# Performance work log

Measured on AMD Instinct MI355X. Metric: run time of the kernel, lower is better.

Reference implementation:

```python
import jax, jax.numpy as jnp
import numpy as np

IN_DIM = 256
OUT_DIM = 64
N = 8192
ALPHA = 0.2  # LeakyReLU negative slope
NEG_BIG = -9e15


def setup_inputs() -> dict:
    key = jax.random.key(0)
    k_h, k_A, k_W, k_a = jax.random.split(key, 4)
    h = jax.random.normal(k_h, (N, IN_DIM), dtype=jnp.float32)
    A = jax.random.randint(k_A, (N, N), 0, 2, dtype=jnp.int32)
    # xavier_uniform with gain=1.414
    gain = 1.414
    lim_W = gain * np.sqrt(6.0 / (IN_DIM + OUT_DIM))
    W = jax.random.uniform(k_W, (IN_DIM, OUT_DIM), minval=-lim_W, maxval=lim_W, dtype=jnp.float32)
    lim_a = gain * np.sqrt(6.0 / (2 * OUT_DIM + 1))
    a = jax.random.uniform(k_a, (2 * OUT_DIM, 1), minval=-lim_a, maxval=lim_a, dtype=jnp.float32)
    return {"h": h, "A": A, "W": W, "a": a}


def reference(h, A, W, a):
    # Wh: [N, d]
    Wh = h @ W
    # e_ij = leakyrelu([Wh_i || Wh_j] . a) = leakyrelu(Wh_i.a1 + Wh_j.a2)
    # -> avoid the O(N^2 * 2d) concat; compute rank-1 decomposition directly.
    a1 = a[:OUT_DIM, 0]   # [d]
    a2 = a[OUT_DIM:, 0]   # [d]
    f1 = Wh @ a1          # [N] contribution of source node i
    f2 = Wh @ a2          # [N] contribution of target node j
    e = jax.nn.leaky_relu(f1[:, None] + f2[None, :], negative_slope=ALPHA)  # [N, N]
    e = jnp.where(A > 0, e, NEG_BIG)
    attention = jax.nn.softmax(e, axis=1)  # [N, N]
    # dropout=0.0 (eval mode): identity
    h_prime = attention @ Wh               # [N, d]
    return jax.nn.elu(h_prime)             # concat=True -> ELU
```

## Files before the change

### kernel.cpp

```cpp
#include <hip/hip_runtime.h>
#include <math.h>
#include <stdint.h>

#define NV 8192
#define KD 256
#define DD 64
#define ALPHA 0.2f
#define TI 64
#define CJ 128
#define BLK 512

typedef _Float16 half8 __attribute__((ext_vector_type(8)));
typedef float floatx4 __attribute__((ext_vector_type(4)));

#define OFF_WHT  0
#define OFF_F1   (DD * NV / 2)
#define OFF_F2   (OFF_F1 + NV)
#define OFF_PACC (OFF_F2 + NV)

__global__ __launch_bounds__(256) void gat_pre(
    const float* __restrict__ h, const float* __restrict__ W,
    const float* __restrict__ a, ushort* __restrict__ whT,
    float* __restrict__ f1, float* __restrict__ f2) {
  __shared__ float hrow[16][KD];
  __shared__ ushort tw[DD][20];
  const int tid = threadIdx.x;
  const int i0 = blockIdx.x * 16;
#pragma unroll
  for (int u = 0; u < 4; ++u) {
    const int idx = tid + u * 256;
    const int row = idx >> 6, col = (idx & 63) * 4;
    *(float4*)&hrow[row][col] = *(const float4*)&h[(long long)(i0 + row) * KD + col];
  }
  __syncthreads();
  const int d = tid & 63;
  const int rg = tid >> 6;
  float wh[4] = {0.f, 0.f, 0.f, 0.f};
#pragma unroll 4
  for (int c = 0; c < KD; ++c) {
    const float wc = W[c * DD + d];
#pragma unroll
    for (int r = 0; r < 4; ++r) wh[r] += hrow[rg * 4 + r][c] * wc;
  }
  const float a1 = a[d], a2 = a[DD + d];
#pragma unroll
  for (int r = 0; r < 4; ++r) {
    float p1 = wh[r] * a1, p2 = wh[r] * a2;
#pragma unroll
    for (int off = 32; off > 0; off >>= 1) {
      p1 += __shfl_down(p1, off);
      p2 += __shfl_down(p2, off);
    }
    if (d == 0) { f1[i0 + rg * 4 + r] = p1; f2[i0 + rg * 4 + r] = p2; }
    union { _Float16 hf; ushort u; } cv;
    cv.hf = (_Float16)wh[r];
    tw[d][rg * 4 + r] = cv.u;
  }
  __syncthreads();
  if (tid < 128) {
    const int dd = tid >> 1, hf = tid & 1;
    *(uint4*)&whT[(long long)dd * NV + i0 + hf * 8] = *(uint4*)&tw[dd][hf * 8];
  }
}

__global__ __launch_bounds__(BLK) void gat_main(
    const int* __restrict__ A, const ushort* __restrict__ whT,
    const float* __restrict__ f1, const float* __restrict__ f2,
    float* __restrict__ pacc, float* __restrict__ pl, int S) {
  __shared__ __align__(16) ushort w_lds[TI * CJ];
  __shared__ __align__(16) ushort b_lds[TI * CJ];
  __shared__ float f1_lds[TI], M_lds[TI], redf[8];

  const int tid = threadIdx.x;
  const int wave = tid >> 6, lane = tid & 63;
  const int tile = blockIdx.x & 127;
  const int s = blockIdx.x >> 7;
  const int i0 = tile * TI;
  const int jrange = NV / S;
  const int j0 = s * jrange;

  float m = -1e30f;
#pragma unroll
  for (int q = 0; q < 16; ++q) m = fmaxf(m, f2[tid + q * BLK]);
#pragma unroll
  for (int off = 32; off > 0; off >>= 1) m = fmaxf(m, __shfl_down(m, off));
  if (lane == 0) redf[wave] = m;
  __syncthreads();
  if (tid < TI) {
    float mm = redf[0];
#pragma unroll
    for (int k = 1; k < 8; ++k) mm = fmaxf(mm, redf[k]);
    float v = f1[i0 + tid];
    f1_lds[tid] = v;
    float x = v + mm;
    M_lds[tid] = x > 0.f ? x : ALPHA * x;
  }

  const int c4 = (tid & 31) * 4;
  const int k8w = (tid & 31) >> 1;
  const int sub = (tid & 1) * 8;
  const int rb = tid >> 5;
  const int bn0 = tid >> 4, bc0 = tid & 15;
  const int bn1 = (tid + BLK) >> 4, bc1 = tid & 15;
  const int mt = wave >> 1;
  const int nt0 = (wave & 1) * 2;
  const int m_ = lane & 15, quad = lane >> 4;

  floatx4 acc0 = {0.f, 0.f, 0.f, 0.f}, acc1 = {0.f, 0.f, 0.f, 0.f};
  float lp[4] = {0.f, 0.f, 0.f, 0.f};

  int4 a_cur[4], a_nxt[4];
  uint4 b_cur[2], b_nxt[2];
  float4 f2_cur, f2_nxt;

  {
    const int jb = j0;
#pragma unroll
    for (int p = 0; p < 4; ++p)
      a_cur[p] = *(const int4*)(A + (long long)(i0 + rb + 16 * p) * NV + jb + c4);
    b_cur[0] = *(const uint4*)(whT + (long long)bn0 * NV + jb + 8 * (bc0 ^ (bn0 & 15)));
    b_cur[1] = *(const uint4*)(whT + (long long)bn1 * NV + jb + 8 * (bc1 ^ (bn1 & 15)));
    f2_cur = *(const float4*)(f2 + jb + c4);
  }

  const int nch = jrange / CJ;
  for (int ch = 0; ch < nch; ++ch) {
    if (ch + 1 < nch) {
      const int jb = j0 + (ch + 1) * CJ;
#pragma unroll
      for (int p = 0; p < 4; ++p)
        a_nxt[p] = *(const int4*)(A + (long long)(i0 + rb + 16 * p) * NV + jb + c4);
      b_nxt[0] = *(const uint4*)(whT + (long long)bn0 * NV + jb + 8 * (bc0 ^ (bn0 & 15)));
      b_nxt[1] = *(const uint4*)(whT + (long long)bn1 * NV + jb + 8 * (bc1 ^ (bn1 & 15)));
      f2_nxt = *(const float4*)(f2 + jb + c4);
    }
    __syncthreads();

    *(uint4*)&b_lds[(tid) * 8] = b_cur[0];
    *(uint4*)&b_lds[(tid + BLK) * 8] = b_cur[1];

#pragma unroll
    for (int p = 0; p < 4; ++p) {
      const int r = rb + 16 * p;
      const int4 a4 = a_cur[p];
      const float f1r = f1_lds[r], Mr = M_lds[r];
      float w0, w1, w2, w3;
      { float x = f1r + f2_cur.x; x = x > 0.f ? x : ALPHA * x; w0 = (a4.x > 0) ? __expf(x - Mr) : 0.f; }
      { float x = f1r + f2_cur.y; x = x > 0.f ? x : ALPHA * x; w1 = (a4.y > 0) ? __expf(x - Mr) : 0.f; }
      { float x = f1r + f2_cur.z; x = x > 0.f ? x : ALPHA * x; w2 = (a4.z > 0) ? __expf(x - Mr) : 0.f; }
      { float x = f1r + f2_cur.w; x = x > 0.f ? x : ALPHA * x; w3 = (a4.w > 0) ? __expf(x - Mr) : 0.f; }
      union { _Float16 hf[4]; uint2 u2; } pk;
      pk.hf[0] = (_Float16)w0; pk.hf[1] = (_Float16)w1;
      pk.hf[2] = (_Float16)w2; pk.hf[3] = (_Float16)w3;
      lp[p] += (float)pk.hf[0] + (float)pk.hf[1] + (float)pk.hf[2] + (float)pk.hf[3];
      *(uint2*)((char*)w_lds + (r * 16 + (k8w ^ (r & 15))) * 16 + sub) = pk.u2;
    }
    __syncthreads();

#pragma unroll
    for (int ks = 0; ks < 4; ++ks) {
      const int cc = 4 * ks + quad;
      const half8 af = *(const half8*)((const char*)w_lds + (((16 * mt + m_) * 16) + (cc ^ m_)) * 16);
      const half8 b0 = *(const half8*)((const char*)b_lds + (((16 * nt0 + m_) * 16) + (cc ^ m_)) * 16);
      const half8 b1 = *(const half8*)((const char*)b_lds + (((16 * (nt0 + 1) + m_) * 16) + (cc ^ m_)) * 16);
      acc0 = __builtin_amdgcn_mfma_f32_16x16x32_f16(af, b0, acc0, 0, 0, 0);
      acc1 = __builtin_amdgcn_mfma_f32_16x16x32_f16(af, b1, acc1, 0, 0, 0);
    }

#pragma unroll
    for (int p = 0; p < 4; ++p) a_cur[p] = a_nxt[p];
    b_cur[0] = b_nxt[0]; b_cur[1] = b_nxt[1];
    f2_cur = f2_nxt;
  }

#pragma unroll
  for (int p = 0; p < 4; ++p) {
    float v = lp[p];
    v += __shfl_down(v, 16, 32);
    v += __shfl_down(v, 8, 32);
    v += __shfl_down(v, 4, 32);
    v += __shfl_down(v, 2, 32);
    v += __shfl_down(v, 1, 32);
    if ((tid & 31) == 0) pl[(long long)s * NV + i0 + rb + 16 * p] = v;
  }

#pragma unroll
  for (int reg = 0; reg < 4; ++reg) {
    const int i = i0 + 16 * mt + quad * 4 + reg;
    const long long base = ((long long)s * NV + i) * DD + m_;
    pacc[base + 16 * nt0] = acc0[reg];
    pacc[base + 16 * (nt0 + 1)] = acc1[reg];
  }
}

__global__ __launch_bounds__(256) void gat_fin(const float* __restrict__ pacc,
                                               const float* __restrict__ pl,
                                               float* __restrict__ out, int S) {
  const int idx = blockIdx.x * 256 + threadIdx.x;
  const int i = idx >> 6;
  float sum = 0.f, l = 0.f;
  for (int q = 0; q < S; ++q) sum += pacc[(long long)q * (NV * DD) + idx];
  for (int q = 0; q < S; ++q) l += pl[q * NV + i];
  const float v = sum / l;
  out[idx] = v > 0.f ? v : expm1f(v);
}

extern "C" void kernel_launch(void* const* d_in, const int* in_sizes, int n_in,
                              void* d_out, int out_size, void* d_ws, size_t ws_size,
                              hipStream_t stream) {
  const float* h = (const float*)d_in[0];
  const int* A = (const int*)d_in[1];
  const float* W = (const float*)d_in[2];
  const float* a = (const float*)d_in[3];
  float* out = (float*)d_out;
  float* ws = (float*)d_ws;

  ushort* whT = (ushort*)(ws + OFF_WHT);
  float* f1 = ws + OFF_F1;
  float* f2 = ws + OFF_F2;
  float* pacc = ws + OFF_PACC;

  int S = 8;
  while (S > 1 &&
         (size_t)(OFF_PACC + (size_t)S * (NV * DD + NV)) * sizeof(float) > ws_size)
    S >>= 1;
  float* pl = pacc + (size_t)S * NV * DD;

  gat_pre<<<NV / 16, 256, 0, stream>>>(h, W, a, whT, f1, f2);
  gat_main<<<(NV / TI) * S, BLK, 0, stream>>>(A, whT, f1, f2, pacc, pl, S);
  gat_fin<<<NV * DD / 256, 256, 0, stream>>>(pacc, pl, out, S);
}
```

Baseline: 460.4 us.

## Build MFMA operands in registers directly from global, dropping LDS staging

Restructures the main attention kernel so that each wave owns 16 rows. Each lane computes its masked softmax weights for its own MFMA A-fragment slot straight from global adjacency loads. The value fragments are also loaded directly from global, so the per-chunk LDS writes and both __syncthreads in the loop go away, and each wave runs its own register double-buffered stream. The block shrinks to 256 threads with a waves-per-EU hint, and only the f2 slice is staged in LDS. It also hard-codes the split count to 8 and drops the workspace-size check. That could overflow a small workspace, and value-fragment reuse now relies on the caches instead of LDS.

```diff
diff --git a/kernel.cpp b/kernel.cpp
--- a/kernel.cpp
+++ b/kernel.cpp
@@ -7,8 +7,8 @@
 #define DD 64
 #define ALPHA 0.2f
 #define TI 64
-#define CJ 128
-#define BLK 512
+#define SPLIT 8
+#define BLK 256
 
 typedef _Float16 half8 __attribute__((ext_vector_type(8)));
 typedef float floatx4 __attribute__((ext_vector_type(4)));
@@ -63,16 +63,17 @@
   }
 }
 
-__global__ __launch_bounds__(BLK) void gat_main(
+__global__ __launch_bounds__(BLK) __attribute__((amdgpu_waves_per_eu(4, 8)))
+void gat_main(
     const int* __restrict__ A, const ushort* __restrict__ whT,
     const float* __restrict__ f1, const float* __restrict__ f2,
     float* __restrict__ pacc, float* __restrict__ pl, int S) {
-  __shared__ __align__(16) ushort w_lds[TI * CJ];
-  __shared__ __align__(16) ushort b_lds[TI * CJ];
-  __shared__ float f1_lds[TI], M_lds[TI], redf[8];
+  __shared__ float f2_lds[NV / SPLIT];
+  __shared__ float redf[4];
 
   const int tid = threadIdx.x;
   const int wave = tid >> 6, lane = tid & 63;
+  const int m_ = lane & 15, quad = lane >> 4;
   const int tile = blockIdx.x & 127;
   const int s = blockIdx.x >> 7;
   const int i0 = tile * TI;
@@ -81,115 +82,83 @@
 
   float m = -1e30f;
 #pragma unroll
-  for (int q = 0; q < 16; ++q) m = fmaxf(m, f2[tid + q * BLK]);
+  for (int q = 0; q < NV / BLK; ++q) m = fmaxf(m, f2[tid + q * BLK]);
 #pragma unroll
   for (int off = 32; off > 0; off >>= 1) m = fmaxf(m, __shfl_down(m, off));
   if (lane == 0) redf[wave] = m;
+
+  for (int u = tid * 4; u < jrange; u += BLK * 4)
+    *(float4*)&f2_lds[u] = *(const float4*)&f2[j0 + u];
   __syncthreads();
-  if (tid < TI) {
-    float mm = redf[0];
+
+  const float mm = fmaxf(fmaxf(redf[0], redf[1]), fmaxf(redf[2], redf[3]));
+  const int row = i0 + wave * 16 + m_;
+  const float f1r = f1[row];
+  const float xm = f1r + mm;
+  const float Mr = fmaxf(xm, ALPHA * xm);
+
+  floatx4 acc[4];
 #pragma unroll
-    for (int k = 1; k < 8; ++k) mm = fmaxf(mm, redf[k]);
-    float v = f1[i0 + tid];
-    f1_lds[tid] = v;
-    float x = v + mm;
-    M_lds[tid] = x > 0.f ? x : ALPHA * x;
+  for (int nt = 0; nt < 4; ++nt) acc[nt] = (floatx4){0.f, 0.f, 0.f, 0.f};
+  float lp = 0.f;
+
+  const int* Arow = A + (long long)row * NV + j0 + quad * 8;
+  const ushort* Bb = whT + j0 + quad * 8;
+
+  int4 aC0 = *(const int4*)(Arow);
+  int4 aC1 = *(const int4*)(Arow + 4);
+  half8 bC[4];
+#pragma unroll
+  for (int nt = 0; nt < 4; ++nt)
+    bC[nt] = *(const half8*)(Bb + (long long)(nt * 16 + m_) * NV);
+
+  for (int kb = 0; kb < jrange; kb += 32) {
+    const int nxt = (kb + 32 < jrange) ? kb + 32 : 0;
+    int4 aN0 = *(const int4*)(Arow + nxt);
+    int4 aN1 = *(const int4*)(Arow + nxt + 4);
+    half8 bN[4];
+#pragma unroll
+    for (int nt = 0; nt < 4; ++nt)
+      bN[nt] = *(const half8*)(Bb + (long long)(nt * 16 + m_) * NV + nxt);
+
+    const int kk = kb + quad * 8;
+    const float4 q0 = *(const float4*)&f2_lds[kk];
+    const float4 q1 = *(const float4*)&f2_lds[kk + 4];
+
+    union { _Float16 hf[8]; half8 v; } wf;
+#define WELT(slot, aval, f2val)                                        \
+    { float x = f1r + (f2val); x = fmaxf(x, ALPHA * x);                \
+      float w = ((aval) > 0) ? __expf(x - Mr) : 0.f;                   \
+      wf.hf[slot] = (_Float16)w; lp += (float)wf.hf[slot]; }
+    WELT(0, aC0.x, q0.x) WELT(1, aC0.y, q0.y)
+    WELT(2, aC0.z, q0.z) WELT(3, aC0.w, q0.w)
+    WELT(4, aC1.x, q1.x) WELT(5, aC1.y, q1.y)
+    WELT(6, aC1.z, q1.z) WELT(7, aC1.w, q1.w)
+#undef WELT
+
+    acc[0] = __builtin_amdgcn_mfma_f32_16x16x32_f16(wf.v, bC[0], acc[0], 0, 0, 0);
+    acc[1] = __builtin_amdgcn_mfma_f32_16x16x32_f16(wf.v, bC[1], acc[1], 0, 0, 0);
+    acc[2] = __builtin_amdgcn_mfma_f32_16x16x32_f16(wf.v, bC[2], acc[2], 0, 0, 0);
+    acc[3] = __builtin_amdgcn_mfma_f32_16x16x32_f16(wf.v, bC[3], acc[3], 0, 0, 0);
+
+    aC0 = aN0; aC1 = aN1;
+#pragma unroll
+    for (int nt = 0; nt < 4; ++nt) bC[nt] = bN[nt];
   }
 
-  const int c4 = (tid & 31) * 4;
-  const int k8w = (tid & 31) >> 1;
-  const int sub = (tid & 1) * 8;
-  const int rb = tid >> 5;
-  const int bn0 = tid >> 4, bc0 = tid & 15;
-  const int bn1 = (tid + BLK) >> 4, bc1 = tid & 15;
-  const int mt = wave >> 1;
-  const int nt0 = (wave & 1) * 2;
-  const int m_ = lane & 15, quad = lane >> 4;
-
-  floatx4 acc0 = {0.f, 0.f, 0.f, 0.f}, acc1 = {0.f, 0.f, 0.f, 0.f};
-  float lp[4] = {0.f, 0.f, 0.f, 0.f};
-
-  int4 a_cur[4], a_nxt[4];
-  uint4 b_cur[2], b_nxt[2];
-  float4 f2_cur, f2_nxt;
-
   {
-    const int jb = j0;
-#pragma unroll
-    for (int p = 0; p < 4; ++p)
-      a_cur[p] = *(const int4*)(A + (long long)(i0 + rb + 16 * p) * NV + jb + c4);
-    b_cur[0] = *(const uint4*)(whT + (long long)bn0 * NV + jb + 8 * (bc0 ^ (bn0 & 15)));
-    b_cur[1] = *(const uint4*)(whT + (long long)bn1 * NV + jb + 8 * (bc1 ^ (bn1 & 15)));
-    f2_cur = *(const float4*)(f2 + jb + c4);
-  }
-
-  const int nch = jrange / CJ;
-  for (int ch = 0; ch < nch; ++ch) {
-    if (ch + 1 < nch) {
-      const int jb = j0 + (ch + 1) * CJ;
-#pragma unroll
-      for (int p = 0; p < 4; ++p)
-        a_nxt[p] = *(const int4*)(A + (long long)(i0 + rb + 16 * p) * NV + jb + c4);
-      b_nxt[0] = *(const uint4*)(whT + (long long)bn0 * NV + jb + 8 * (bc0 ^ (bn0 & 15)));
-      b_nxt[1] = *(const uint4*)(whT + (long long)bn1 * NV + jb + 8 * (bc1 ^ (bn1 & 15)));
-      f2_nxt = *(const float4*)(f2 + jb + c4);
-    }
-    __syncthreads();
-
-    *(uint4*)&b_lds[(tid) * 8] = b_cur[0];
-    *(uint4*)&b_lds[(tid + BLK) * 8] = b_cur[1];
-
-#pragma unroll
-    for (int p = 0; p < 4; ++p) {
-      const int r = rb + 16 * p;
-      const int4 a4 = a_cur[p];
-      const float f1r = f1_lds[r], Mr = M_lds[r];
-      float w0, w1, w2, w3;
-      { float x = f1r + f2_cur.x; x = x > 0.f ? x : ALPHA * x; w0 = (a4.x > 0) ? __expf(x - Mr) : 0.f; }
-      { float x = f1r + f2_cur.y; x = x > 0.f ? x : ALPHA * x; w1 = (a4.y > 0) ? __expf(x - Mr) : 0.f; }
-      { float x = f1r + f2_cur.z; x = x > 0.f ? x : ALPHA * x; w2 = (a4.z > 0) ? __expf(x - Mr) : 0.f; }
-      { float x = f1r + f2_cur.w; x = x > 0.f ? x : ALPHA * x; w3 = (a4.w > 0) ? __expf(x - Mr) : 0.f; }
-      union { _Float16 hf[4]; uint2 u2; } pk;
-      pk.hf[0] = (_Float16)w0; pk.hf[1] = (_Float16)w1;
-      pk.hf[2] = (_Float16)w2; pk.hf[3] = (_Float16)w3;
-      lp[p] += (float)pk.hf[0] + (float)pk.hf[1] + (float)pk.hf[2] + (float)pk.hf[3];
-      *(uint2*)((char*)w_lds + (r * 16 + (k8w ^ (r & 15))) * 16 + sub) = pk.u2;
-    }
-    __syncthreads();
-
-#pragma unroll
-    for (int ks = 0; ks < 4; ++ks) {
-      const int cc = 4 * ks + quad;
-      const half8 af = *(const half8*)((const char*)w_lds + (((16 * mt + m_) * 16) + (cc ^ m_)) * 16);
-      const half8 b0 = *(const half8*)((const char*)b_lds + (((16 * nt0 + m_) * 16) + (cc ^ m_)) * 16);
-      const half8 b1 = *(const half8*)((const char*)b_lds + (((16 * (nt0 + 1) + m_) * 16) + (cc ^ m_)) * 16);
-      acc0 = __builtin_amdgcn_mfma_f32_16x16x32_f16(af, b0, acc0, 0, 0, 0);
-      acc1 = __builtin_amdgcn_mfma_f32_16x16x32_f16(af, b1, acc1, 0, 0, 0);
-    }
-
-#pragma unroll
-    for (int p = 0; p < 4; ++p) a_cur[p] = a_nxt[p];
-    b_cur[0] = b_nxt[0]; b_cur[1] = b_nxt[1];
-    f2_cur = f2_nxt;
-  }
-
-#pragma unroll
-  for (int p = 0; p < 4; ++p) {
-    float v = lp[p];
-    v += __shfl_down(v, 16, 32);
-    v += __shfl_down(v, 8, 32);
-    v += __shfl_down(v, 4, 32);
-    v += __shfl_down(v, 2, 32);
-    v += __shfl_down(v, 1, 32);
-    if ((tid & 31) == 0) pl[(long long)s * NV + i0 + rb + 16 * p] = v;
+    float v = lp;
+    v += __shfl_down(v, 32);
+    v += __shfl_down(v, 16);
+    if (lane < 16) pl[(long long)s * NV + row] = v;
   }
 
 #pragma unroll
   for (int reg = 0; reg < 4; ++reg) {
-    const int i = i0 + 16 * mt + quad * 4 + reg;
+    const int i = i0 + wave * 16 + quad * 4 + reg;
     const long long base = ((long long)s * NV + i) * DD + m_;
-    pacc[base + 16 * nt0] = acc0[reg];
-    pacc[base + 16 * (nt0 + 1)] = acc1[reg];
+#pragma unroll
+    for (int nt = 0; nt < 4; ++nt) pacc[base + 16 * nt] = acc[nt][reg];
   }
 }
 
@@ -220,10 +189,7 @@
   float* f2 = ws + OFF_F2;
   float* pacc = ws + OFF_PACC;
 
-  int S = 8;
-  while (S > 1 &&
-         (size_t)(OFF_PACC + (size_t)S * (NV * DD + NV)) * sizeof(float) > ws_size)
-    S >>= 1;
+  const int S = SPLIT;
   float* pl = pacc + (size_t)S * NV * DD;
 
   gat_pre<<<NV / 16, 256, 0, stream>>>(h, W, a, whT, f1, f2);
```

Result: no change. 456.9 us (-0.8%).

## Precompute softmax row bound in separate kernel and drop register prefetching

Applied to the files above, without the earlier changes.

Moves the global f2 max reduction and per-row bound M into a new single-block kernel, so each main block no longer rereads all of f2. It also removes the register double-buffered prefetch of A, whT and f2 and loads them inside the loop, which lowers register pressure but exposes memory latency unless occupancy hides it. The split count is fixed at 8 without checking workspace size, and the LeakyReLU select becomes fmaxf.

```diff
diff --git a/kernel.cpp b/kernel.cpp
--- a/kernel.cpp
+++ b/kernel.cpp
@@ -8,6 +8,7 @@
 #define ALPHA 0.2f
 #define TI 64
 #define CJ 128
+#define SPLIT 8
 #define BLK 512
 
 typedef _Float16 half8 __attribute__((ext_vector_type(8)));
@@ -16,7 +17,8 @@
 #define OFF_WHT  0
 #define OFF_F1   (DD * NV / 2)
 #define OFF_F2   (OFF_F1 + NV)
-#define OFF_PACC (OFF_F2 + NV)
+#define OFF_M    (OFF_F2 + NV)
+#define OFF_PACC (OFF_M + NV)
 
 __global__ __launch_bounds__(256) void gat_pre(
     const float* __restrict__ h, const float* __restrict__ W,
@@ -63,13 +65,32 @@
   }
 }
 
+__global__ __launch_bounds__(256) void gat_maxm(
+    const float* __restrict__ f1, const float* __restrict__ f2,
+    float* __restrict__ M) {
+  __shared__ float red[4];
+  const int tid = threadIdx.x;
+  float m = -1e30f;
+  for (int j = tid; j < NV; j += 256) m = fmaxf(m, f2[j]);
+#pragma unroll
+  for (int off = 32; off > 0; off >>= 1) m = fmaxf(m, __shfl_down(m, off));
+  if ((tid & 63) == 0) red[tid >> 6] = m;
+  __syncthreads();
+  const float mm = fmaxf(fmaxf(red[0], red[1]), fmaxf(red[2], red[3]));
+  for (int i = tid; i < NV; i += 256) {
+    const float x = f1[i] + mm;
+    M[i] = fmaxf(x, ALPHA * x);
+  }
+}
+
 __global__ __launch_bounds__(BLK) void gat_main(
     const int* __restrict__ A, const ushort* __restrict__ whT,
-    const float* __restrict__ f1, const float* __restrict__ f2,
-    float* __restrict__ pacc, float* __restrict__ pl, int S) {
+    const float* __restrict__ f1, const float* __restrict__ Mv,
+    const float* __restrict__ f2, float* __restrict__ pacc,
+    float* __restrict__ pl, int S) {
   __shared__ __align__(16) ushort w_lds[TI * CJ];
   __shared__ __align__(16) ushort b_lds[TI * CJ];
-  __shared__ float f1_lds[TI], M_lds[TI], redf[8];
+  __shared__ float f1_lds[TI], M_lds[TI];
 
   const int tid = threadIdx.x;
   const int wave = tid >> 6, lane = tid & 63;
@@ -79,29 +100,15 @@
   const int jrange = NV / S;
   const int j0 = s * jrange;
 
-  float m = -1e30f;
-#pragma unroll
-  for (int q = 0; q < 16; ++q) m = fmaxf(m, f2[tid + q * BLK]);
-#pragma unroll
-  for (int off = 32; off > 0; off >>= 1) m = fmaxf(m, __shfl_down(m, off));
-  if (lane == 0) redf[wave] = m;
-  __syncthreads();
   if (tid < TI) {
-    float mm = redf[0];
-#pragma unroll
-    for (int k = 1; k < 8; ++k) mm = fmaxf(mm, redf[k]);
-    float v = f1[i0 + tid];
-    f1_lds[tid] = v;
-    float x = v + mm;
-    M_lds[tid] = x > 0.f ? x : ALPHA * x;
+    f1_lds[tid] = f1[i0 + tid];
+    M_lds[tid] = Mv[i0 + tid];
   }
 
   const int c4 = (tid & 31) * 4;
   const int k8w = (tid & 31) >> 1;
   const int sub = (tid & 1) * 8;
   const int rb = tid >> 5;
-  const int bn0 = tid >> 4, bc0 = tid & 15;
-  const int bn1 = (tid + BLK) >> 4, bc1 = tid & 15;
   const int mt = wave >> 1;
   const int nt0 = (wave & 1) * 2;
   const int m_ = lane & 15, quad = lane >> 4;
@@ -109,46 +116,30 @@
   floatx4 acc0 = {0.f, 0.f, 0.f, 0.f}, acc1 = {0.f, 0.f, 0.f, 0.f};
   float lp[4] = {0.f, 0.f, 0.f, 0.f};
 
-  int4 a_cur[4], a_nxt[4];
-  uint4 b_cur[2], b_nxt[2];
-  float4 f2_cur, f2_nxt;
-
-  {
-    const int jb = j0;
-#pragma unroll
-    for (int p = 0; p < 4; ++p)
-      a_cur[p] = *(const int4*)(A + (long long)(i0 + rb + 16 * p) * NV + jb + c4);
-    b_cur[0] = *(const uint4*)(whT + (long long)bn0 * NV + jb + 8 * (bc0 ^ (bn0 & 15)));
-    b_cur[1] = *(const uint4*)(whT + (long long)bn1 * NV + jb + 8 * (bc1 ^ (bn1 & 15)));
-    f2_cur = *(const float4*)(f2 + jb + c4);
-  }
-
   const int nch = jrange / CJ;
   for (int ch = 0; ch < nch; ++ch) {
-    if (ch + 1 < nch) {
-      const int jb = j0 + (ch + 1) * CJ;
-#pragma unroll
-      for (int p = 0; p < 4; ++p)
-        a_nxt[p] = *(const int4*)(A + (long long)(i0 + rb + 16 * p) * NV + jb + c4);
-      b_nxt[0] = *(const uint4*)(whT + (long long)bn0 * NV + jb + 8 * (bc0 ^ (bn0 & 15)));
-      b_nxt[1] = *(const uint4*)(whT + (long long)bn1 * NV + jb + 8 * (bc1 ^ (bn1 & 15)));
-      f2_nxt = *(const float4*)(f2 + jb + c4);
-    }
+    const int jb = j0 + ch * CJ;
     __syncthreads();
 
-    *(uint4*)&b_lds[(tid) * 8] = b_cur[0];
-    *(uint4*)&b_lds[(tid + BLK) * 8] = b_cur[1];
-
+#pragma unroll
+    for (int u = 0; u < 2; ++u) {
+      const int idx = tid + u * BLK;
+      const int n = idx >> 4, c = idx & 15;
+      const uint4 t = *(const uint4*)(whT + (long long)n * NV + jb + 8 * (c ^ (n & 15)));
+      *(uint4*)&b_lds[idx * 8] = t;
+    }
+
+    const float4 f2v = *(const float4*)(f2 + jb + c4);
 #pragma unroll
     for (int p = 0; p < 4; ++p) {
       const int r = rb + 16 * p;
-      const int4 a4 = a_cur[p];
+      const int4 a4 = *(const int4*)(A + (long long)(i0 + r) * NV + jb + c4);
       const float f1r = f1_lds[r], Mr = M_lds[r];
       float w0, w1, w2, w3;
-      { float x = f1r + f2_cur.x; x = x > 0.f ? x : ALPHA * x; w0 = (a4.x > 0) ? __expf(x - Mr) : 0.f; }
-      { float x = f1r + f2_cur.y; x = x > 0.f ? x : ALPHA * x; w1 = (a4.y > 0) ? __expf(x - Mr) : 0.f; }
-      { float x = f1r + f2_cur.z; x = x > 0.f ? x : ALPHA * x; w2 = (a4.z > 0) ? __expf(x - Mr) : 0.f; }
-      { float x = f1r + f2_cur.w; x = x > 0.f ? x : ALPHA * x; w3 = (a4.w > 0) ? __expf(x - Mr) : 0.f; }
+      { float x = f1r + f2v.x; x = fmaxf(x, ALPHA * x); w0 = (a4.x > 0) ? __expf(x - Mr) : 0.f; }
+      { float x = f1r + f2v.y; x = fmaxf(x, ALPHA * x); w1 = (a4.y > 0) ? __expf(x - Mr) : 0.f; }
+      { float x = f1r + f2v.z; x = fmaxf(x, ALPHA * x); w2 = (a4.z > 0) ? __expf(x - Mr) : 0.f; }
+      { float x = f1r + f2v.w; x = fmaxf(x, ALPHA * x); w3 = (a4.w > 0) ? __expf(x - Mr) : 0.f; }
       union { _Float16 hf[4]; uint2 u2; } pk;
       pk.hf[0] = (_Float16)w0; pk.hf[1] = (_Float16)w1;
       pk.hf[2] = (_Float16)w2; pk.hf[3] = (_Float16)w3;
@@ -166,11 +157,6 @@
       acc0 = __builtin_amdgcn_mfma_f32_16x16x32_f16(af, b0, acc0, 0, 0, 0);
       acc1 = __builtin_amdgcn_mfma_f32_16x16x32_f16(af, b1, acc1, 0, 0, 0);
     }
-
-#pragma unroll
-    for (int p = 0; p < 4; ++p) a_cur[p] = a_nxt[p];
-    b_cur[0] = b_nxt[0]; b_cur[1] = b_nxt[1];
-    f2_cur = f2_nxt;
   }
 
 #pragma unroll
@@ -218,15 +204,14 @@
   ushort* whT = (ushort*)(ws + OFF_WHT);
   float* f1 = ws + OFF_F1;
   float* f2 = ws + OFF_F2;
+  float* Mv = ws + OFF_M;
   float* pacc = ws + OFF_PACC;
 
-  int S = 8;
-  while (S > 1 &&
-         (size_t)(OFF_PACC + (size_t)S * (NV * DD + NV)) * sizeof(float) > ws_size)
-    S >>= 1;
+  const int S = SPLIT;
   float* pl = pacc + (size_t)S * NV * DD;
 
   gat_pre<<<NV / 16, 256, 0, stream>>>(h, W, a, whT, f1, f2);
-  gat_main<<<(NV / TI) * S, BLK, 0, stream>>>(A, whT, f1, f2, pacc, pl, S);
+  gat_maxm<<<1, 256, 0, stream>>>(f1, f2, Mv);
+  gat_main<<<(NV / TI) * S, BLK, 0, stream>>>(A, whT, f1, Mv, f2, pacc, pl, S);
   gat_fin<<<NV * DD / 256, 256, 0, stream>>>(pacc, pl, out, S);
 }
```

Measured after the change: 432.4 us. -6.1%, faster.
